# Kernel optimization log

Hardware: AMD Instinct MI355X
Metric: run time of the kernel (lower is better)

Reference implementation:

```python
import jax, jax.numpy as jnp
import numpy as np

B, T, E = 2, 2048, 1024
H = 16
D = E // H  # 64

def setup_inputs() -> dict:
    key = jax.random.key(0)
    kx, kq, kk, kv, ko = jax.random.split(key, 5)
    s = 1.0 / np.sqrt(E)
    return {
        "x":  jax.random.normal(kx, (B, T, E), dtype=jnp.float32),
        "Wq": jax.random.normal(kq, (E, E), dtype=jnp.float32) * s,
        "Wk": jax.random.normal(kk, (E, E), dtype=jnp.float32) * s,
        "Wv": jax.random.normal(kv, (E, E), dtype=jnp.float32) * s,
        "Wo": jax.random.normal(ko, (E, E), dtype=jnp.float32) * s,
    }

def reference(x, Wq, Wk, Wv, Wo):
    # Faithful to the torch module, including its quirks:
    #  - head split is a raw .view(B, H, T, D) reshape (NOT a transpose split)
    #  - masked_fill result is discarded in the original, so NO causal mask is applied
    #  - dropout = 0.0 -> identity
    b, t, e = x.shape
    q = jnp.reshape(x @ Wq, (b, H, t, D))
    k = jnp.reshape(x @ Wk, (b, H, t, D))
    v = jnp.reshape(x @ Wv, (b, H, t, D))
    # raw_score = q @ k^T ; softmax over keys of raw_score / sqrt(head_dim)
    scores = jnp.einsum("bhtd,bhsd->bhts", q, k) / jnp.sqrt(jnp.asarray(D, x.dtype))
    attn = jax.nn.softmax(scores, axis=-1)
    h = jnp.einsum("bhts,bhsd->bhtd", attn, v)           # (B,H,T,D)
    h = jnp.reshape(h, (b, t, e))                         # .view(B, T, -1)
    return h @ Wo
```

## Files before the change

kernel.cpp:

```cpp
#include <hip/hip_runtime.h>
#include <hip/hip_bf16.h>
#include <math.h>

#define BB 2
#define TT 2048
#define EE 1024
#define HH 16
#define DD 64
#define MM (BB*TT)

typedef __bf16 bf16;
typedef bf16 bf16x8 __attribute__((ext_vector_type(8)));
typedef bf16 bf16x4 __attribute__((ext_vector_type(4)));
typedef bf16 bf16x2 __attribute__((ext_vector_type(2)));
typedef float f32x4 __attribute__((ext_vector_type(4)));

#define MFMA16(a,b,c) __builtin_amdgcn_mfma_f32_16x16x32_bf16((a),(b),(c),0,0,0)

__device__ __forceinline__ void gload_lds16(const void* g, void* l) {
  __builtin_amdgcn_global_load_lds(
      (const __attribute__((address_space(1))) unsigned int*)g,
      (__attribute__((address_space(3))) unsigned int*)l, 16, 0, 0);
}

__device__ __forceinline__ unsigned short bits(bf16 h) {
  return __builtin_bit_cast(unsigned short, h);
}

__global__ __launch_bounds__(256) void cvt_bf16(const float* __restrict__ in,
                                                bf16* __restrict__ out, int n4) {
  int i = blockIdx.x * blockDim.x + threadIdx.x;
  if (i < n4) {
    float4 f = ((const float4*)in)[i];
    bf16x4 h;
    h[0] = (bf16)f.x; h[1] = (bf16)f.y; h[2] = (bf16)f.z; h[3] = (bf16)f.w;
    ((bf16x4*)out)[i] = h;
  }
}

__global__ __launch_bounds__(256) void transpose_cvt4(const float* __restrict__ w0,
                                                      const float* __restrict__ w1,
                                                      const float* __restrict__ w2,
                                                      const float* __restrict__ w3,
                                                      bf16* t0, bf16* t1, bf16* t2, bf16* t3) {
  const float* W = blockIdx.z == 0 ? w0 : blockIdx.z == 1 ? w1 : blockIdx.z == 2 ? w2 : w3;
  bf16* T = blockIdx.z == 0 ? t0 : blockIdx.z == 1 ? t1 : blockIdx.z == 2 ? t2 : t3;
  __shared__ bf16 tile[64][65];
  const int n0 = blockIdx.x * 64, k0 = blockIdx.y * 64;
#pragma unroll
  for (int i = 0; i < 16; i++) {
    int idx = threadIdx.x + i * 256;
    int r = idx >> 6, c = idx & 63;
    tile[c][r] = (bf16)W[(size_t)(k0 + r) * EE + n0 + c];
  }
  __syncthreads();
#pragma unroll
  for (int i = 0; i < 16; i++) {
    int idx = threadIdx.x + i * 256;
    int r = idx >> 6, c = idx & 63;
    T[(size_t)(n0 + r) * EE + k0 + c] = tile[r][c];
  }
}

template <typename OutT>
__device__ __forceinline__ void gemm_core(const bf16* __restrict__ A, const bf16* __restrict__ Bt,
                                          OutT* __restrict__ C, bf16* As, bf16* Bs) {
  const int tid = threadIdx.x;
  const int w = tid >> 6, lane = tid & 63;
  const int lg = lane >> 4, lr = lane & 15;
  const int row0 = blockIdx.y * 128, col0 = blockIdx.x * 128;
  const int wrow = (w >> 1) * 64, wcol = (w & 1) * 64;
  f32x4 acc[4][4];
#pragma unroll
  for (int m = 0; m < 4; m++)
#pragma unroll
    for (int n = 0; n < 4; n++) acc[m][n] = f32x4{0.f, 0.f, 0.f, 0.f};

  for (int kt = 0; kt < EE; kt += 32) {
#pragma unroll
    for (int i = 0; i < 2; i++) {
      const int c = i * 4 + w;
      const int row = c * 16 + (lane >> 2);
      const int kof = (lane & 3) * 8;
      gload_lds16(A + (size_t)(row0 + row) * EE + kt + kof, &As[c * 512]);
      gload_lds16(Bt + (size_t)(col0 + row) * EE + kt + kof, &Bs[c * 512]);
    }
    __syncthreads();
    bf16x8 a[4], b[4];
#pragma unroll
    for (int m = 0; m < 4; m++)
      a[m] = *(const bf16x8*)&As[(wrow + m * 16 + lr) * 32 + lg * 8];
#pragma unroll
    for (int n = 0; n < 4; n++)
      b[n] = *(const bf16x8*)&Bs[(wcol + n * 16 + lr) * 32 + lg * 8];
#pragma unroll
    for (int m = 0; m < 4; m++)
#pragma unroll
      for (int n = 0; n < 4; n++) acc[m][n] = MFMA16(a[m], b[n], acc[m][n]);
    __syncthreads();
  }
#pragma unroll
  for (int m = 0; m < 4; m++)
#pragma unroll
    for (int n = 0; n < 4; n++)
#pragma unroll
      for (int r = 0; r < 4; r++) {
        const int rr = row0 + wrow + m * 16 + lg * 4 + r;
        const int cc = col0 + wcol + n * 16 + lr;
        C[(size_t)rr * EE + cc] = (OutT)acc[m][n][r];
      }
}

__global__ __launch_bounds__(256) void gemm_qkv(const bf16* __restrict__ A,
                                                const bf16* __restrict__ w0,
                                                const bf16* __restrict__ w1,
                                                const bf16* __restrict__ w2,
                                                bf16* o0, bf16* o1, bf16* o2) {
  __shared__ __align__(16) bf16 As[128 * 32];
  __shared__ __align__(16) bf16 Bs[128 * 32];
  const bf16* Bt = (blockIdx.z == 0) ? w0 : (blockIdx.z == 1) ? w1 : w2;
  bf16* C = (blockIdx.z == 0) ? o0 : (blockIdx.z == 1) ? o1 : o2;
  gemm_core<bf16>(A, Bt, C, As, Bs);
}

__global__ __launch_bounds__(256) void gemm_out(const bf16* __restrict__ A,
                                                const bf16* __restrict__ Bt,
                                                float* __restrict__ C) {
  __shared__ __align__(16) bf16 As[128 * 32];
  __shared__ __align__(16) bf16 Bs[128 * 32];
  gemm_core<float>(A, Bt, C, As, Bs);
}

__global__ __launch_bounds__(512, 4) void flash_attn(const bf16* __restrict__ Q,
                                                     const bf16* __restrict__ K,
                                                     const bf16* __restrict__ V,
                                                     bf16* __restrict__ Hout) {
  const int tid = threadIdx.x;
  const int w = tid >> 6, lane = tid & 63;
  const int hi = lane >> 4, lr = lane & 15;

  const int bid = blockIdx.x + 16 * blockIdx.y;
  const int sid = (bid & 7) * 64 + (bid >> 3);
  const int qb = sid & 15, bh = sid >> 4;

  const size_t base = (size_t)(bh >> 4) * TT * EE + (size_t)(bh & 15) * 128 * EE;
  const bf16* qh = Q + base;
  const bf16* kh = K + base;
  const bf16* vh = V + base;
  bf16* hh = Hout + base;
  const int r0w = qb * 128 + w * 16;

  __shared__ __align__(16) bf16 Ks[2][64 * 72];
  __shared__ __align__(16) bf16 Vt[2][64 * 72];
  __shared__ __align__(16) bf16 Ps[8 * 16 * 72];
  bf16* Pw = &Ps[w * 16 * 72];

  const float qscale = 0.18033688011112042f;
  bf16x8 aq[2];
#pragma unroll
  for (int kk = 0; kk < 2; kk++) {
    bf16x8 qv = *(const bf16x8*)(qh + (size_t)(r0w + lr) * DD + kk * 32 + hi * 8);
#pragma unroll
    for (int j = 0; j < 8; j++) qv[j] = (bf16)(qscale * (float)qv[j]);
    aq[kk] = qv;
  }

  float l_ = 0.f;
  f32x4 o[4];
#pragma unroll
  for (int d = 0; d < 4; d++) o[d] = f32x4{0.f, 0.f, 0.f, 0.f};

  const int ks_s = tid >> 3, ks_d = (tid & 7) * 8;
  const int vsp = tid & 31, vdb = (tid >> 5) * 4;

  bf16x8 kreg = *(const bf16x8*)(kh + (size_t)ks_s * DD + ks_d);
  bf16x4 va = *(const bf16x4*)(vh + (size_t)(2 * vsp) * DD + vdb);
  bf16x4 vb2 = *(const bf16x4*)(vh + (size_t)(2 * vsp + 1) * DD + vdb);
  *(bf16x8*)&Ks[0][ks_s * 72 + ks_d] = kreg;
#pragma unroll
  for (int j = 0; j < 4; j++) {
    unsigned u = (unsigned)bits(va[j]) | ((unsigned)bits(vb2[j]) << 16);
    *(unsigned*)&Vt[0][(vdb + j) * 72 + 2 * vsp] = u;
  }
  kreg = *(const bf16x8*)(kh + (size_t)(64 + ks_s) * DD + ks_d);
  va = *(const bf16x4*)(vh + (size_t)(64 + 2 * vsp) * DD + vdb);
  vb2 = *(const bf16x4*)(vh + (size_t)(64 + 2 * vsp + 1) * DD + vdb);
  __syncthreads();

  for (int t = 0; t < TT / 64; t++) {
    const bf16* Kc = Ks[t & 1];
    const bf16* Vc = Vt[t & 1];

    f32x4 sA[4];
#pragma unroll
    for (int cf = 0; cf < 4; cf++) sA[cf] = f32x4{0.f, 0.f, 0.f, 0.f};
#pragma unroll
    for (int cf = 0; cf < 4; cf++)
#pragma unroll
      for (int kk = 0; kk < 2; kk++) {
        bf16x8 bk = *(const bf16x8*)&Kc[(cf * 16 + lr) * 72 + kk * 32 + hi * 8];
        sA[cf] = MFMA16(bk, aq[kk], sA[cf]);
      }

#pragma unroll
    for (int cf = 0; cf < 4; cf++) {
      bf16x4 pb;
#pragma unroll
      for (int r = 0; r < 4; r++) {
        float p = __builtin_amdgcn_exp2f(sA[cf][r]);
        l_ += p;
        pb[r] = (bf16)p;
      }
      *(bf16x4*)&Pw[lr * 72 + cf * 16 + 4 * hi] = pb;
    }
    asm volatile("s_waitcnt lgkmcnt(0)" ::: "memory");

#pragma unroll
    for (int kk = 0; kk < 2; kk++) {
      bf16x8 bp = *(const bf16x8*)&Pw[lr * 72 + kk * 32 + hi * 8];
#pragma unroll
      for (int dblk = 0; dblk < 4; dblk++) {
        bf16x8 av = *(const bf16x8*)&Vc[(dblk * 16 + lr) * 72 + kk * 32 + hi * 8];
        o[dblk] = MFMA16(av, bp, o[dblk]);
      }
    }

    if (t < TT / 64 - 1) {
      bf16* Kn = Ks[(t + 1) & 1];
      bf16* Vn = Vt[(t + 1) & 1];
      *(bf16x8*)&Kn[ks_s * 72 + ks_d] = kreg;
#pragma unroll
      for (int j = 0; j < 4; j++) {
        unsigned u = (unsigned)bits(va[j]) | ((unsigned)bits(vb2[j]) << 16);
        *(unsigned*)&Vn[(vdb + j) * 72 + 2 * vsp] = u;
      }
      if (t < TT / 64 - 2) {
        const int s2 = (t + 2) * 64;
        kreg = *(const bf16x8*)(kh + (size_t)(s2 + ks_s) * DD + ks_d);
        va = *(const bf16x4*)(vh + (size_t)(s2 + 2 * vsp) * DD + vdb);
        vb2 = *(const bf16x4*)(vh + (size_t)(s2 + 2 * vsp + 1) * DD + vdb);
      }
    }
    __syncthreads();
  }

  float lt = l_;
  lt += __shfl_xor(lt, 16);
  lt += __shfl_xor(lt, 32);
#pragma unroll
  for (int dblk = 0; dblk < 4; dblk++) {
    bf16x4 st;
#pragma unroll
    for (int r = 0; r < 4; r++) st[r] = (bf16)(o[dblk][r] / lt);
    *(bf16x4*)(hh + (size_t)(r0w + lr) * DD + dblk * 16 + 4 * hi) = st;
  }
}

extern "C" void kernel_launch(void* const* d_in, const int* in_sizes, int n_in,
                              void* d_out, int out_size, void* d_ws, size_t ws_size,
                              hipStream_t stream) {
  const float* x  = (const float*)d_in[0];
  const float* Wq = (const float*)d_in[1];
  const float* Wk = (const float*)d_in[2];
  const float* Wv = (const float*)d_in[3];
  const float* Wo = (const float*)d_in[4];
  float* out = (float*)d_out;

  bf16* xb  = (bf16*)d_ws;
  bf16* wqt = xb + (size_t)MM * EE;
  bf16* wkt = wqt + (size_t)EE * EE;
  bf16* wvt = wkt + (size_t)EE * EE;
  bf16* wot = wvt + (size_t)EE * EE;
  bf16* Qb  = wot + (size_t)EE * EE;
  bf16* Kb  = Qb + (size_t)MM * EE;
  bf16* Vb  = Kb + (size_t)MM * EE;
  bf16* Hb  = xb;

  cvt_bf16<<<dim3(MM * EE / 1024), 256, 0, stream>>>(x, xb, MM * EE / 4);
  transpose_cvt4<<<dim3(16, 16, 4), 256, 0, stream>>>(Wq, Wk, Wv, Wo, wqt, wkt, wvt, wot);
  gemm_qkv<<<dim3(8, 32, 3), 256, 0, stream>>>(xb, wqt, wkt, wvt, Qb, Kb, Vb);
  flash_attn<<<dim3(16, 32), 512, 0, stream>>>(Qb, Kb, Vb, Hb);
  gemm_out<<<dim3(8, 32), 256, 0, stream>>>(Hb, wot, out);
}
```

Baseline: 126.7 us.

## Give each attention wave two query row groups and merge prep kernels

The flash attention kernel now runs 256 threads per block, and each wave handles 32 query rows (two 16-row groups) instead of 16. Each K and V fragment read from LDS now feeds two MFMAs, which halves LDS traffic per FLOP. Each thread also loads twice as much K/V per tile into shared memory. Separately, the x conversion and the weight transpose kernels are fused into one launch. The cost is more registers per thread and fewer waves available to hide latency.

```diff
diff --git a/kernel.cpp b/kernel.cpp
--- a/kernel.cpp
+++ b/kernel.cpp
@@ -12,7 +12,6 @@
 typedef __bf16 bf16;
 typedef bf16 bf16x8 __attribute__((ext_vector_type(8)));
 typedef bf16 bf16x4 __attribute__((ext_vector_type(4)));
-typedef bf16 bf16x2 __attribute__((ext_vector_type(2)));
 typedef float f32x4 __attribute__((ext_vector_type(4)));
 
 #define MFMA16(a,b,c) __builtin_amdgcn_mfma_f32_16x16x32_bf16((a),(b),(c),0,0,0)
@@ -27,26 +26,28 @@
   return __builtin_bit_cast(unsigned short, h);
 }
 
-__global__ __launch_bounds__(256) void cvt_bf16(const float* __restrict__ in,
-                                                bf16* __restrict__ out, int n4) {
-  int i = blockIdx.x * blockDim.x + threadIdx.x;
-  if (i < n4) {
-    float4 f = ((const float4*)in)[i];
+__global__ __launch_bounds__(256) void prep(const float* __restrict__ x,
+                                            const float* __restrict__ w0,
+                                            const float* __restrict__ w1,
+                                            const float* __restrict__ w2,
+                                            const float* __restrict__ w3,
+                                            bf16* __restrict__ xb,
+                                            bf16* t0, bf16* t1, bf16* t2, bf16* t3) {
+  __shared__ bf16 tile[64][65];
+  const int bid = blockIdx.x;
+  if (bid < 4096) {
+    const int i = bid * 256 + threadIdx.x;
+    float4 f = ((const float4*)x)[i];
     bf16x4 h;
     h[0] = (bf16)f.x; h[1] = (bf16)f.y; h[2] = (bf16)f.z; h[3] = (bf16)f.w;
-    ((bf16x4*)out)[i] = h;
-  }
-}
-
-__global__ __launch_bounds__(256) void transpose_cvt4(const float* __restrict__ w0,
-                                                      const float* __restrict__ w1,
-                                                      const float* __restrict__ w2,
-                                                      const float* __restrict__ w3,
-                                                      bf16* t0, bf16* t1, bf16* t2, bf16* t3) {
-  const float* W = blockIdx.z == 0 ? w0 : blockIdx.z == 1 ? w1 : blockIdx.z == 2 ? w2 : w3;
-  bf16* T = blockIdx.z == 0 ? t0 : blockIdx.z == 1 ? t1 : blockIdx.z == 2 ? t2 : t3;
-  __shared__ bf16 tile[64][65];
-  const int n0 = blockIdx.x * 64, k0 = blockIdx.y * 64;
+    ((bf16x4*)xb)[i] = h;
+    return;
+  }
+  const int t = bid - 4096;
+  const int z = t >> 8, rem = t & 255;
+  const float* W = z == 0 ? w0 : z == 1 ? w1 : z == 2 ? w2 : w3;
+  bf16* T = z == 0 ? t0 : z == 1 ? t1 : z == 2 ? t2 : t3;
+  const int n0 = (rem & 15) * 64, k0 = (rem >> 4) * 64;
 #pragma unroll
   for (int i = 0; i < 16; i++) {
     int idx = threadIdx.x + i * 256;
@@ -131,7 +132,7 @@
   gemm_core<float>(A, Bt, C, As, Bs);
 }
 
-__global__ __launch_bounds__(512, 4) void flash_attn(const bf16* __restrict__ Q,
+__global__ __launch_bounds__(256, 2) void flash_attn(const bf16* __restrict__ Q,
                                                      const bf16* __restrict__ K,
                                                      const bf16* __restrict__ V,
                                                      bf16* __restrict__ Hout) {
@@ -148,111 +149,143 @@
   const bf16* kh = K + base;
   const bf16* vh = V + base;
   bf16* hh = Hout + base;
-  const int r0w = qb * 128 + w * 16;
+  const int r0w = qb * 128 + w * 32;
 
   __shared__ __align__(16) bf16 Ks[2][64 * 72];
   __shared__ __align__(16) bf16 Vt[2][64 * 72];
-  __shared__ __align__(16) bf16 Ps[8 * 16 * 72];
-  bf16* Pw = &Ps[w * 16 * 72];
+  __shared__ __align__(16) bf16 Ps[4 * 32 * 72];
+  bf16* Pw = &Ps[w * 32 * 72];
 
   const float qscale = 0.18033688011112042f;
-  bf16x8 aq[2];
-#pragma unroll
-  for (int kk = 0; kk < 2; kk++) {
-    bf16x8 qv = *(const bf16x8*)(qh + (size_t)(r0w + lr) * DD + kk * 32 + hi * 8);
-#pragma unroll
-    for (int j = 0; j < 8; j++) qv[j] = (bf16)(qscale * (float)qv[j]);
-    aq[kk] = qv;
-  }
-
-  float l_ = 0.f;
-  f32x4 o[4];
-#pragma unroll
-  for (int d = 0; d < 4; d++) o[d] = f32x4{0.f, 0.f, 0.f, 0.f};
-
-  const int ks_s = tid >> 3, ks_d = (tid & 7) * 8;
+  bf16x8 aq[2][2];
+#pragma unroll
+  for (int rg = 0; rg < 2; rg++)
+#pragma unroll
+    for (int kk = 0; kk < 2; kk++) {
+      bf16x8 qv = *(const bf16x8*)(qh + (size_t)(r0w + rg * 16 + lr) * DD + kk * 32 + hi * 8);
+#pragma unroll
+      for (int j = 0; j < 8; j++) qv[j] = (bf16)(qscale * (float)qv[j]);
+      aq[rg][kk] = qv;
+    }
+
+  float l_[2] = {0.f, 0.f};
+  f32x4 o[2][4];
+#pragma unroll
+  for (int rg = 0; rg < 2; rg++)
+#pragma unroll
+    for (int d = 0; d < 4; d++) o[rg][d] = f32x4{0.f, 0.f, 0.f, 0.f};
+
+  const int krow = tid >> 2, kg8 = (tid & 3) * 8;
   const int vsp = tid & 31, vdb = (tid >> 5) * 4;
 
-  bf16x8 kreg = *(const bf16x8*)(kh + (size_t)ks_s * DD + ks_d);
-  bf16x4 va = *(const bf16x4*)(vh + (size_t)(2 * vsp) * DD + vdb);
-  bf16x4 vb2 = *(const bf16x4*)(vh + (size_t)(2 * vsp + 1) * DD + vdb);
-  *(bf16x8*)&Ks[0][ks_s * 72 + ks_d] = kreg;
+  bf16x8 kr0 = *(const bf16x8*)(kh + (size_t)krow * DD + kg8);
+  bf16x8 kr1 = *(const bf16x8*)(kh + (size_t)krow * DD + kg8 + 32);
+  bf16x4 va0 = *(const bf16x4*)(vh + (size_t)(2 * vsp) * DD + vdb);
+  bf16x4 vb0 = *(const bf16x4*)(vh + (size_t)(2 * vsp + 1) * DD + vdb);
+  bf16x4 va1 = *(const bf16x4*)(vh + (size_t)(2 * vsp) * DD + vdb + 32);
+  bf16x4 vb1 = *(const bf16x4*)(vh + (size_t)(2 * vsp + 1) * DD + vdb + 32);
+  *(bf16x8*)&Ks[0][krow * 72 + kg8] = kr0;
+  *(bf16x8*)&Ks[0][krow * 72 + kg8 + 32] = kr1;
 #pragma unroll
   for (int j = 0; j < 4; j++) {
-    unsigned u = (unsigned)bits(va[j]) | ((unsigned)bits(vb2[j]) << 16);
-    *(unsigned*)&Vt[0][(vdb + j) * 72 + 2 * vsp] = u;
-  }
-  kreg = *(const bf16x8*)(kh + (size_t)(64 + ks_s) * DD + ks_d);
-  va = *(const bf16x4*)(vh + (size_t)(64 + 2 * vsp) * DD + vdb);
-  vb2 = *(const bf16x4*)(vh + (size_t)(64 + 2 * vsp + 1) * DD + vdb);
+    unsigned u0 = (unsigned)bits(va0[j]) | ((unsigned)bits(vb0[j]) << 16);
+    unsigned u1 = (unsigned)bits(va1[j]) | ((unsigned)bits(vb1[j]) << 16);
+    *(unsigned*)&Vt[0][(vdb + j) * 72 + 2 * vsp] = u0;
+    *(unsigned*)&Vt[0][(vdb + 32 + j) * 72 + 2 * vsp] = u1;
+  }
+  kr0 = *(const bf16x8*)(kh + (size_t)(64 + krow) * DD + kg8);
+  kr1 = *(const bf16x8*)(kh + (size_t)(64 + krow) * DD + kg8 + 32);
+  va0 = *(const bf16x4*)(vh + (size_t)(64 + 2 * vsp) * DD + vdb);
+  vb0 = *(const bf16x4*)(vh + (size_t)(64 + 2 * vsp + 1) * DD + vdb);
+  va1 = *(const bf16x4*)(vh + (size_t)(64 + 2 * vsp) * DD + vdb + 32);
+  vb1 = *(const bf16x4*)(vh + (size_t)(64 + 2 * vsp + 1) * DD + vdb + 32);
   __syncthreads();
 
   for (int t = 0; t < TT / 64; t++) {
     const bf16* Kc = Ks[t & 1];
     const bf16* Vc = Vt[t & 1];
 
-    f32x4 sA[4];
-#pragma unroll
-    for (int cf = 0; cf < 4; cf++) sA[cf] = f32x4{0.f, 0.f, 0.f, 0.f};
+    f32x4 sA[2][4];
+#pragma unroll
+    for (int rg = 0; rg < 2; rg++)
+#pragma unroll
+      for (int cf = 0; cf < 4; cf++) sA[rg][cf] = f32x4{0.f, 0.f, 0.f, 0.f};
 #pragma unroll
     for (int cf = 0; cf < 4; cf++)
 #pragma unroll
       for (int kk = 0; kk < 2; kk++) {
         bf16x8 bk = *(const bf16x8*)&Kc[(cf * 16 + lr) * 72 + kk * 32 + hi * 8];
-        sA[cf] = MFMA16(bk, aq[kk], sA[cf]);
-      }
-
-#pragma unroll
-    for (int cf = 0; cf < 4; cf++) {
-      bf16x4 pb;
-#pragma unroll
-      for (int r = 0; r < 4; r++) {
-        float p = __builtin_amdgcn_exp2f(sA[cf][r]);
-        l_ += p;
-        pb[r] = (bf16)p;
-      }
-      *(bf16x4*)&Pw[lr * 72 + cf * 16 + 4 * hi] = pb;
-    }
+#pragma unroll
+        for (int rg = 0; rg < 2; rg++) sA[rg][cf] = MFMA16(bk, aq[rg][kk], sA[rg][cf]);
+      }
+
+#pragma unroll
+    for (int rg = 0; rg < 2; rg++)
+#pragma unroll
+      for (int cf = 0; cf < 4; cf++) {
+        bf16x4 pb;
+#pragma unroll
+        for (int r = 0; r < 4; r++) {
+          float p = __builtin_amdgcn_exp2f(sA[rg][cf][r]);
+          l_[rg] += p;
+          pb[r] = (bf16)p;
+        }
+        *(bf16x4*)&Pw[(rg * 16 + lr) * 72 + cf * 16 + 4 * hi] = pb;
+      }
     asm volatile("s_waitcnt lgkmcnt(0)" ::: "memory");
 
 #pragma unroll
     for (int kk = 0; kk < 2; kk++) {
-      bf16x8 bp = *(const bf16x8*)&Pw[lr * 72 + kk * 32 + hi * 8];
+      bf16x8 bp[2];
+#pragma unroll
+      for (int rg = 0; rg < 2; rg++)
+        bp[rg] = *(const bf16x8*)&Pw[(rg * 16 + lr) * 72 + kk * 32 + hi * 8];
 #pragma unroll
       for (int dblk = 0; dblk < 4; dblk++) {
         bf16x8 av = *(const bf16x8*)&Vc[(dblk * 16 + lr) * 72 + kk * 32 + hi * 8];
-        o[dblk] = MFMA16(av, bp, o[dblk]);
+#pragma unroll
+        for (int rg = 0; rg < 2; rg++)
+          o[rg][dblk] = MFMA16(av, bp[rg], o[rg][dblk]);
       }
     }
 
     if (t < TT / 64 - 1) {
       bf16* Kn = Ks[(t + 1) & 1];
       bf16* Vn = Vt[(t + 1) & 1];
-      *(bf16x8*)&Kn[ks_s * 72 + ks_d] = kreg;
+      *(bf16x8*)&Kn[krow * 72 + kg8] = kr0;
+      *(bf16x8*)&Kn[krow * 72 + kg8 + 32] = kr1;
 #pragma unroll
       for (int j = 0; j < 4; j++) {
-        unsigned u = (unsigned)bits(va[j]) | ((unsigned)bits(vb2[j]) << 16);
-        *(unsigned*)&Vn[(vdb + j) * 72 + 2 * vsp] = u;
+        unsigned u0 = (unsigned)bits(va0[j]) | ((unsigned)bits(vb0[j]) << 16);
+        unsigned u1 = (unsigned)bits(va1[j]) | ((unsigned)bits(vb1[j]) << 16);
+        *(unsigned*)&Vn[(vdb + j) * 72 + 2 * vsp] = u0;
+        *(unsigned*)&Vn[(vdb + 32 + j) * 72 + 2 * vsp] = u1;
       }
       if (t < TT / 64 - 2) {
         const int s2 = (t + 2) * 64;
-        kreg = *(const bf16x8*)(kh + (size_t)(s2 + ks_s) * DD + ks_d);
-        va = *(const bf16x4*)(vh + (size_t)(s2 + 2 * vsp) * DD + vdb);
-        vb2 = *(const bf16x4*)(vh + (size_t)(s2 + 2 * vsp + 1) * DD + vdb);
+        kr0 = *(const bf16x8*)(kh + (size_t)(s2 + krow) * DD + kg8);
+        kr1 = *(const bf16x8*)(kh + (size_t)(s2 + krow) * DD + kg8 + 32);
+        va0 = *(const bf16x4*)(vh + (size_t)(s2 + 2 * vsp) * DD + vdb);
+        vb0 = *(const bf16x4*)(vh + (size_t)(s2 + 2 * vsp + 1) * DD + vdb);
+        va1 = *(const bf16x4*)(vh + (size_t)(s2 + 2 * vsp) * DD + vdb + 32);
+        vb1 = *(const bf16x4*)(vh + (size_t)(s2 + 2 * vsp + 1) * DD + vdb + 32);
       }
     }
     __syncthreads();
   }
 
-  float lt = l_;
-  lt += __shfl_xor(lt, 16);
-  lt += __shfl_xor(lt, 32);
-#pragma unroll
-  for (int dblk = 0; dblk < 4; dblk++) {
-    bf16x4 st;
-#pragma unroll
-    for (int r = 0; r < 4; r++) st[r] = (bf16)(o[dblk][r] / lt);
-    *(bf16x4*)(hh + (size_t)(r0w + lr) * DD + dblk * 16 + 4 * hi) = st;
+#pragma unroll
+  for (int rg = 0; rg < 2; rg++) {
+    float lt = l_[rg];
+    lt += __shfl_xor(lt, 16);
+    lt += __shfl_xor(lt, 32);
+#pragma unroll
+    for (int dblk = 0; dblk < 4; dblk++) {
+      bf16x4 st;
+#pragma unroll
+      for (int r = 0; r < 4; r++) st[r] = (bf16)(o[rg][dblk][r] / lt);
+      *(bf16x4*)(hh + (size_t)(r0w + rg * 16 + lr) * DD + dblk * 16 + 4 * hi) = st;
+    }
   }
 }
 
@@ -276,9 +309,8 @@
   bf16* Vb  = Kb + (size_t)MM * EE;
   bf16* Hb  = xb;
 
-  cvt_bf16<<<dim3(MM * EE / 1024), 256, 0, stream>>>(x, xb, MM * EE / 4);
-  transpose_cvt4<<<dim3(16, 16, 4), 256, 0, stream>>>(Wq, Wk, Wv, Wo, wqt, wkt, wvt, wot);
+  prep<<<dim3(5120), 256, 0, stream>>>(x, Wq, Wk, Wv, Wo, xb, wqt, wkt, wvt, wot);
   gemm_qkv<<<dim3(8, 32, 3), 256, 0, stream>>>(xb, wqt, wkt, wvt, Qb, Kb, Vb);
-  flash_attn<<<dim3(16, 32), 512, 0, stream>>>(Qb, Kb, Vb, Hb);
+  flash_attn<<<dim3(16, 32), 256, 0, stream>>>(Qb, Kb, Vb, Hb);
   gemm_out<<<dim3(8, 32), 256, 0, stream>>>(Hb, wot, out);
 }
```

Result: faster. 122.3 us (-3.5%).
